# Optimization experiments

Hardware: AMD Instinct MI355X
Metric: run time of the kernel (lower is better)

## Reference

```python
import jax, jax.numpy as jnp
import numpy as np

NUM_HEADS = 16
WINDOW_SIZE = (7, 7, 7)  # (D, H, W)


def _relative_position_index(window_size):
    # Faithful numpy replication of SwinWindowAttention.get_relative_position_index (3D branch).
    D, H, W = window_size
    w, d, h = np.meshgrid(np.arange(W), np.arange(D), np.arange(H), indexing='ij')
    coords = np.stack([d, h, w], axis=0)              # [3, W, D, H]
    flat = coords.reshape(3, -1)                       # [3, N]
    rel = flat[:, :, None] - flat[:, None, :]          # [3, N, N]
    rel = rel.transpose(1, 2, 0)                       # [N, N, 3]
    offsets = []
    mult = 1
    for size in reversed(window_size):
        offsets.insert(0, mult)
        mult *= 2 * size - 1
    offsets = np.asarray(offsets, dtype=np.int32)
    rel = rel + np.asarray([s - 1 for s in window_size])
    return np.sum(rel.astype(np.int32) * offsets, axis=-1).astype(np.int32)  # [N, N]


def setup_inputs() -> dict:
    key = jax.random.key(0)
    ks = jax.random.split(key, 6)
    B, N, C = 64, 343, 512          # B = true_batch * num_windows
    NW = 8                           # mask_size; B % NW == 0
    TBL = 13 * 13 * 13              # prod(2*s - 1) = 2197
    x = jax.random.normal(ks[0], (B, N, C), dtype=jnp.float32)
    mask = jnp.zeros((NW, N, N), dtype=jnp.float32)  # shift mask (0 / -inf pattern in practice)
    w_qkv = jax.random.normal(ks[1], (C, 3 * C), dtype=jnp.float32) * (C ** -0.5)
    b_qkv = jnp.zeros((3 * C,), dtype=jnp.float32)
    w_proj = jax.random.normal(ks[2], (C, C), dtype=jnp.float32) * (C ** -0.5)
    b_proj = jnp.zeros((C,), dtype=jnp.float32)
    bias_table = jax.random.normal(ks[3], (TBL, NUM_HEADS), dtype=jnp.float32) * 0.02
    rel_index = jnp.asarray(_relative_position_index(WINDOW_SIZE))  # [N, N] int32
    return {"x": x, "mask": mask, "w_qkv": w_qkv, "b_qkv": b_qkv,
            "w_proj": w_proj, "b_proj": b_proj, "bias_table": bias_table,
            "rel_index": rel_index}


def reference(x, mask, w_qkv, b_qkv, w_proj, b_proj, bias_table, rel_index):
    B, N, C = x.shape
    H = NUM_HEADS
    hd = C // H
    scale = hd ** -0.5
    qkv = x @ w_qkv + b_qkv                              # [B, N, 3C]
    qkv = qkv.reshape(B, N, 3, H, hd).transpose(2, 0, 3, 1, 4)  # [3, B, H, N, hd]
    q, k, v = qkv[0] * scale, qkv[1], qkv[2]
    attn = jnp.einsum('bhnd,bhmd->bhnm', q, k)           # [B, H, N, N]
    # relative position bias: gather [N,N,H] -> [H,N,N]
    bias = bias_table[rel_index].transpose(2, 0, 1)
    attn = attn + bias[None]
    nw = mask.shape[0]
    attn = attn.reshape(B // nw, nw, H, N, N) + mask[:, None, :, :]
    attn = attn.reshape(B, H, N, N)
    attn = jax.nn.softmax(attn, axis=-1)
    out = jnp.einsum('bhnm,bhmd->bhnd', attn, v)         # [B, H, N, hd]
    out = out.transpose(0, 2, 1, 3).reshape(B, N, C)
    return out @ w_proj + b_proj
```

## Files before the change

kernel.cpp:

```cpp
#include <hip/hip_runtime.h>

typedef __bf16 bf16_t;
typedef __bf16 bf16x4 __attribute__((ext_vector_type(4)));
typedef __bf16 bf16x8 __attribute__((ext_vector_type(8)));
typedef short  s16x4  __attribute__((ext_vector_type(4)));
typedef float  f32x4  __attribute__((ext_vector_type(4)));

#define NUM_B 64
#define SEQ   343
#define CH    512
#define NH    16
#define HDIM  32
#define NWIN  8
#define C3    1536
#define MTOT  (NUM_B * SEQ)
#define MPAD  22016
#define NTILES 22
#define NPAD  352
#define NN    (SEQ * SEQ)
#define MB_TILES 172
#define QSCALE 0.17677669529663687f
#define LOG2E  1.4426950408889634f

__device__ __forceinline__ f32x4 mfma16(bf16x8 a, bf16x8 b, f32x4 c) {
    return __builtin_amdgcn_mfma_f32_16x16x32_bf16(a, b, c, 0, 0, 0);
}

__device__ __forceinline__ f32x4 mfma16k16(bf16x4 a, bf16x4 b, f32x4 c) {
    return __builtin_amdgcn_mfma_f32_16x16x16bf16_1k(
        __builtin_bit_cast(s16x4, a), __builtin_bit_cast(s16x4, b), c, 0, 0, 0);
}

__device__ __forceinline__ bf16x8 bf8_zero() {
    bf16x8 v;
#pragma unroll
    for (int i = 0; i < 8; ++i) v[i] = (bf16_t)0.f;
    return v;
}

__device__ __forceinline__ bf16x8 pack8(const float4& a, const float4& b) {
    bf16x8 v;
    v[0] = (bf16_t)a.x; v[1] = (bf16_t)a.y; v[2] = (bf16_t)a.z; v[3] = (bf16_t)a.w;
    v[4] = (bf16_t)b.x; v[5] = (bf16_t)b.y; v[6] = (bf16_t)b.z; v[7] = (bf16_t)b.w;
    return v;
}

__device__ __forceinline__ float f4get(const float4& v, int i) {
    return i == 0 ? v.x : i == 1 ? v.y : i == 2 ? v.z : v.w;
}

__device__ __forceinline__ void gload16(const void* g, void* l) {
    __builtin_amdgcn_global_load_lds(
        (const __attribute__((address_space(1))) void*)g,
        (__attribute__((address_space(3))) void*)l, 16, 0, 0);
}

__global__ __launch_bounds__(256) void swin_prep(
        const float* __restrict__ X, const float* __restrict__ Wq,
        const float* __restrict__ Wp, const float* __restrict__ bias_table,
        const int* __restrict__ rel_index, const float* __restrict__ mask,
        bf16_t* __restrict__ Xb, bf16_t* __restrict__ Bfq, bf16_t* __restrict__ Bfp,
        bf16_t* __restrict__ comb) {
    __shared__ __align__(16) float shbuf[32 * 33];
    const int bid = blockIdx.x, t = threadIdx.x;
    if (bid < 5504) {
        size_t e = ((size_t)bid * 256 + t) * 8;
        bf16x8 v;
        if (e < (size_t)MTOT * CH) {
            const float4* p = reinterpret_cast<const float4*>(&X[e]);
            v = pack8(p[0], p[1]);
        } else v = bf8_zero();
        *reinterpret_cast<bf16x8*>(&Xb[e]) = v;
        return;
    }
    if (bid < 6528) {
        float (*tile)[33] = reinterpret_cast<float(*)[33]>(shbuf);
        const float* src; bf16_t* dst; int srcN, k0, n0;
        if (bid < 6272) {
            int b2 = bid - 5504;
            k0 = (b2 % 16) * 32; n0 = (b2 / 16) * 32;
            src = Wq; dst = Bfq; srcN = C3;
        } else {
            int b2 = bid - 6272;
            k0 = (b2 % 16) * 32; n0 = (b2 / 16) * 32;
            src = Wp; dst = Bfp; srcN = CH;
        }
        int r = t >> 3, c4 = (t & 7) * 4;
        const float4 u = *reinterpret_cast<const float4*>(&src[(size_t)(k0 + r) * srcN + n0 + c4]);
        tile[r][c4 + 0] = u.x; tile[r][c4 + 1] = u.y; tile[r][c4 + 2] = u.z; tile[r][c4 + 3] = u.w;
        __syncthreads();
        const int sub = t >> 7, lane2 = (t >> 1) & 63, half = t & 1;
        const int lm = lane2 & 15, g = lane2 >> 4;
        bf16x4 o;
#pragma unroll
        for (int e = 0; e < 4; ++e)
            o[e] = (bf16_t)tile[g * 8 + half * 4 + e][sub * 16 + lm];
        const size_t off = ((size_t)(((n0 >> 4) + sub) * 16 + (k0 >> 5)) * 64 + lane2) * 8 + half * 4;
        *reinterpret_cast<bf16x4*>(&dst[off]) = o;
        return;
    }
    const int cid = bid - 6528;
    const int ntq = cid % 6, mt = (cid / 6) % NTILES, w = cid / (6 * NTILES);
    const int nt = ntq * 4 + (t >> 6);
    if (nt >= NTILES) return;
    const int lane = t & 63;
    const int lm = lane & 15, g = lane >> 4;
    const int gm = mt * 16 + lm;
    const bool gmok = gm < SEQ;

    bool ok[4]; int idx[4]; float mv[4];
#pragma unroll
    for (int r = 0; r < 4; ++r) {
        int gn = nt * 16 + 4 * g + r;
        ok[r] = gmok && (gn < SEQ);
        int a = ok[r] ? gm * SEQ + gn : 0;
        idx[r] = rel_index[a];
        mv[r] = ok[r] ? mask[(size_t)w * NN + a] : 0.f;
    }
    const size_t outb = ((size_t)mt * NTILES + nt) * 64 + lane;
    bf16x4* combv = reinterpret_cast<bf16x4*>(comb);
#pragma unroll
    for (int hq = 0; hq < 4; ++hq) {
        float4 b0 = *reinterpret_cast<const float4*>(&bias_table[idx[0] * NH + hq * 4]);
        float4 b1 = *reinterpret_cast<const float4*>(&bias_table[idx[1] * NH + hq * 4]);
        float4 b2 = *reinterpret_cast<const float4*>(&bias_table[idx[2] * NH + hq * 4]);
        float4 b3 = *reinterpret_cast<const float4*>(&bias_table[idx[3] * NH + hq * 4]);
#pragma unroll
        for (int hh = 0; hh < 4; ++hh) {
            int h = hq * 4 + hh;
            bf16x4 o;
            o[0] = ok[0] ? (bf16_t)((f4get(b0, hh) + mv[0]) * LOG2E) : (bf16_t)(-1e30f);
            o[1] = ok[1] ? (bf16_t)((f4get(b1, hh) + mv[1]) * LOG2E) : (bf16_t)(-1e30f);
            o[2] = ok[2] ? (bf16_t)((f4get(b2, hh) + mv[2]) * LOG2E) : (bf16_t)(-1e30f);
            o[3] = ok[3] ? (bf16_t)((f4get(b3, hh) + mv[3]) * LOG2E) : (bf16_t)(-1e30f);
            combv[(size_t)(h * 8 + w) * (NTILES * NTILES * 64) + outb] = o;
        }
    }
}

template <int NB, bool QKV>
__global__ __launch_bounds__(256) void swin_gemm(
        const bf16_t* __restrict__ A, const bf16_t* __restrict__ Bf,
        const float* __restrict__ bias, void* __restrict__ outv) {
    __shared__ __align__(16) bf16_t shraw[17408];
    const int nwg8 = MB_TILES * NB / 8;
    int bid = blockIdx.x;
    bid = (bid & 7) * nwg8 + (bid >> 3);
    const int nb = bid % NB, mb = bid / NB;
    const int m0 = mb * 128, n0 = nb * 128;
    const int t = threadIdx.x, wid = t >> 6, lane = t & 63;
    const int wr = wid >> 1, wc = wid & 1;
    const int lm = lane & 15, g = lane >> 4;
    const int swr = ((lane >> 2) ^ (lane >> 4)) & 3;
    const bf16_t* gA = &A[(size_t)(m0 + wid * 32 + (lane >> 2)) * CH + (((lane & 3) ^ swr) << 3)];
    const int soff = ((g ^ ((lm ^ (lm >> 2)) & 3)) << 3);
    const bf16_t* gBf = &Bf[((size_t)((n0 >> 4) + wc * 4) * 16) * 512 + lane * 8];

    f32x4 acc[4][4];
#pragma unroll
    for (int i = 0; i < 4; ++i)
#pragma unroll
        for (int j = 0; j < 4; ++j) {
            acc[i][j][0] = 0.f; acc[i][j][1] = 0.f; acc[i][j][2] = 0.f; acc[i][j][3] = 0.f;
        }

#define STAGE(tile, buf)                                                          \
    do {                                                                          \
        const int _k0 = (tile) * 32;                                              \
        gload16(gA + _k0,           &shraw[(buf) * 4096 + (wid * 32 + 0) * 32]);  \
        gload16(gA + _k0 + 16 * CH, &shraw[(buf) * 4096 + (wid * 32 + 16) * 32]); \
    } while (0)

    STAGE(0, 0);
    STAGE(1, 1);
    bf16x8 bc[4], bn[4];
#pragma unroll
    for (int j = 0; j < 4; ++j)
        bc[j] = *reinterpret_cast<const bf16x8*>(gBf + (size_t)j * 8192);

#pragma unroll
    for (int kt = 0; kt < 16; ++kt) {
        if (kt <= 14) asm volatile("s_waitcnt vmcnt(6)" ::: "memory");
        else          asm volatile("s_waitcnt vmcnt(4)" ::: "memory");
        __builtin_amdgcn_s_barrier();
        __builtin_amdgcn_sched_barrier(0);
        if (kt <= 13) STAGE(kt + 2, (kt + 2) % 3);
        if (kt <= 14) {
#pragma unroll
            for (int j = 0; j < 4; ++j)
                bn[j] = *reinterpret_cast<const bf16x8*>(gBf + (size_t)j * 8192 + (kt + 1) * 512);
        }
        const int buf = kt % 3;
        bf16x8 a[4];
#pragma unroll
        for (int i = 0; i < 4; ++i)
            a[i] = *reinterpret_cast<const bf16x8*>(&shraw[buf * 4096 + (wr * 64 + i * 16 + lm) * 32 + soff]);
        __builtin_amdgcn_s_setprio(1);
#pragma unroll
        for (int i = 0; i < 4; ++i)
#pragma unroll
            for (int j = 0; j < 4; ++j)
                acc[i][j] = mfma16(a[i], bc[j], acc[i][j]);
        __builtin_amdgcn_s_setprio(0);
        if (kt <= 14) {
#pragma unroll
            for (int j = 0; j < 4; ++j) bc[j] = bn[j];
        }
    }
#undef STAGE
    __syncthreads();

    const int rb = (lane >> 4) << 2;
    if (QKV) {
        bf16_t* Cs = &shraw[0];
#pragma unroll
        for (int j = 0; j < 4; ++j) {
            int col = wc * 64 + j * 16 + lm;
            float bv = bias[n0 + col];
            float sc = (n0 + col < CH) ? (QSCALE * LOG2E) : 1.0f;
#pragma unroll
            for (int i = 0; i < 4; ++i)
#pragma unroll
                for (int r = 0; r < 4; ++r)
                    Cs[(wr * 64 + i * 16 + rb + r) * 136 + col] = (bf16_t)((acc[i][j][r] + bv) * sc);
        }
        __syncthreads();
        bf16_t* outp = (bf16_t*)outv;
#pragma unroll
        for (int it = 0; it < 8; ++it) {
            int row = (t >> 4) + it * 16;
            int c8 = (t & 15) * 8;
            bf16x8 v = *reinterpret_cast<const bf16x8*>(&Cs[row * 136 + c8]);
            int grow = m0 + row;
            if (grow < MTOT)
                *reinterpret_cast<bf16x8*>(&outp[(size_t)grow * (NB * 128) + n0 + c8]) = v;
        }
    } else {
        float* fCs = reinterpret_cast<float*>(&shraw[0]);
        float* outp = (float*)outv;
#pragma unroll
        for (int half = 0; half < 2; ++half) {
            __syncthreads();
            if (wr == half) {
#pragma unroll
                for (int j = 0; j < 4; ++j) {
                    int col = wc * 64 + j * 16 + lm;
                    float bv = bias[n0 + col];
#pragma unroll
                    for (int i = 0; i < 4; ++i)
#pragma unroll
                        for (int r = 0; r < 4; ++r)
                            fCs[(i * 16 + rb + r) * 128 + col] = acc[i][j][r] + bv;
                }
            }
            __syncthreads();
#pragma unroll
            for (int it = 0; it < 8; ++it) {
                int row = (t >> 5) + it * 8;
                int c4 = (t & 31) * 4;
                float4 v = *reinterpret_cast<const float4*>(&fCs[row * 128 + c4]);
                int grow = m0 + half * 64 + row;
                if (grow < MTOT)
                    *reinterpret_cast<float4*>(&outp[(size_t)grow * (NB * 128) + n0 + c4]) = v;
            }
        }
    }
}

__global__ __launch_bounds__(512, 6) void swin_attn(
        const bf16_t* __restrict__ qkv, const bf16_t* __restrict__ comb,
        bf16_t* __restrict__ attout) {
    __shared__ __align__(16) bf16_t Ksh[NPAD * 32];
    __shared__ __align__(16) bf16_t Vsh[32 * NPAD];
    const int t = threadIdx.x;
    const int bid = blockIdx.x;
    const int h = (bid & 127) >> 3;
    const int w = bid & 7;
    const int b = w + ((bid >> 7) << 3);
    const int plane = h * 8 + w;
    const int wid = t >> 6, lane = t & 63;
    const int lm = lane & 15, g = lane >> 4;
    const int lkb = g << 3;
    const size_t rowbase = (size_t)b * SEQ;

    for (int base = 0; base < SEQ; base += 128) {
        int n = base + (t >> 2);
        int db = (t & 3) << 3;
        if (n < SEQ) {
            bf16x8 kv = *reinterpret_cast<const bf16x8*>(&qkv[(rowbase + n) * C3 + CH + h * HDIM + db]);
            *reinterpret_cast<bf16x8*>(&Ksh[(n * 32 + db) ^ (((n >> 1) & 3) << 3)]) = kv;
            bf16x8 vv = *reinterpret_cast<const bf16x8*>(&qkv[(rowbase + n) * C3 + 2 * CH + h * HDIM + db]);
#pragma unroll
            for (int e = 0; e < 8; ++e) {
                int d = db + e;
                Vsh[(d * NPAD + n) ^ (((d >> 1) & 3) << 3)] = vv[e];
            }
        }
    }
    if (t < 36) {
        int n = SEQ + (t >> 2), db = (t & 3) << 3;
        *reinterpret_cast<bf16x8*>(&Ksh[(n * 32 + db) ^ (((n >> 1) & 3) << 3)]) = bf8_zero();
    }
    for (int i = t; i < 32 * 9; i += 512) {
        int d = i / 9, n = SEQ + (i % 9);
        Vsh[(d * NPAD + n) ^ (((d >> 1) & 3) << 3)] = (bf16_t)0.f;
    }
    __syncthreads();

    const int kswz = ((lm >> 1) & 3) << 3;
    const int kbase = (lm * 32 + lkb) ^ kswz;
    const int vb0e = (lm * NPAD + 4 * g) ^ kswz;
    const int vb0o = (lm * NPAD + 4 * g + 16) ^ kswz;
    const int vb1e = ((16 + lm) * NPAD + 4 * g) ^ kswz;
    const int vb1o = ((16 + lm) * NPAD + 4 * g + 16) ^ kswz;

    bf16x4 ones;
    ones[0] = (bf16_t)1.f; ones[1] = (bf16_t)1.f; ones[2] = (bf16_t)1.f; ones[3] = (bf16_t)1.f;

    {
        const int m0a = wid * 16, m0b = (wid + 8) * 16;
        bf16x8 qfa = *reinterpret_cast<const bf16x8*>(&qkv[(rowbase + m0a + lm) * C3 + h * HDIM + lkb]);
        bf16x8 qfb = *reinterpret_cast<const bf16x8*>(&qkv[(rowbase + m0b + lm) * C3 + h * HDIM + lkb]);

        f32x4 o0a = {0.f, 0.f, 0.f, 0.f}, o1a = {0.f, 0.f, 0.f, 0.f}, osa = {0.f, 0.f, 0.f, 0.f};
        f32x4 o0b = {0.f, 0.f, 0.f, 0.f}, o1b = {0.f, 0.f, 0.f, 0.f}, osb = {0.f, 0.f, 0.f, 0.f};
        const bf16x4* cpa = reinterpret_cast<const bf16x4*>(comb) + ((size_t)plane * NTILES + wid) * NTILES * 64;
        const bf16x4* cpb = reinterpret_cast<const bf16x4*>(comb) + ((size_t)plane * NTILES + wid + 8) * NTILES * 64;
#pragma unroll 2
        for (int nt = 0; nt < NTILES; ++nt) {
            bf16x4 cba = cpa[nt * 64 + lane];
            bf16x4 cbb = cpb[nt * 64 + lane];
            bf16x8 kf = *reinterpret_cast<const bf16x8*>(&Ksh[kbase + nt * 512]);
            f32x4 za, zb;
            za[0] = (float)cba[0]; za[1] = (float)cba[1]; za[2] = (float)cba[2]; za[3] = (float)cba[3];
            zb[0] = (float)cbb[0]; zb[1] = (float)cbb[1]; zb[2] = (float)cbb[2]; zb[3] = (float)cbb[3];
            f32x4 sa = mfma16(kf, qfa, za);
            f32x4 sb = mfma16(kf, qfb, zb);
            bf16x4 paa, pab;
#pragma unroll
            for (int r = 0; r < 4; ++r) {
                paa[r] = (bf16_t)__builtin_amdgcn_exp2f(sa[r]);
                pab[r] = (bf16_t)__builtin_amdgcn_exp2f(sb[r]);
            }
            const int off = (nt >> 1) * 32;
            bf16x4 v0 = *reinterpret_cast<const bf16x4*>(&Vsh[((nt & 1) ? vb0o : vb0e) + off]);
            bf16x4 v1 = *reinterpret_cast<const bf16x4*>(&Vsh[((nt & 1) ? vb1o : vb1e) + off]);
            o0a = mfma16k16(paa, v0, o0a);
            o0b = mfma16k16(pab, v0, o0b);
            o1a = mfma16k16(paa, v1, o1a);
            o1b = mfma16k16(pab, v1, o1b);
            osa = mfma16k16(paa, ones, osa);
            osb = mfma16k16(pab, ones, osb);
        }
#pragma unroll
        for (int r = 0; r < 4; ++r) {
            int gma = m0a + 4 * g + r;
            float iva = 1.f / osa[r];
            attout[(rowbase + gma) * CH + h * HDIM + lm]      = (bf16_t)(o0a[r] * iva);
            attout[(rowbase + gma) * CH + h * HDIM + 16 + lm] = (bf16_t)(o1a[r] * iva);
            int gmb = m0b + 4 * g + r;
            float ivb = 1.f / osb[r];
            attout[(rowbase + gmb) * CH + h * HDIM + lm]      = (bf16_t)(o0b[r] * ivb);
            attout[(rowbase + gmb) * CH + h * HDIM + 16 + lm] = (bf16_t)(o1b[r] * ivb);
        }
    }

    if (wid < 6) {
        const int mt = wid + 16;
        const int m0 = mt * 16;
        bf16x8 qf = *reinterpret_cast<const bf16x8*>(&qkv[(rowbase + m0 + lm) * C3 + h * HDIM + lkb]);

        f32x4 o0 = {0.f, 0.f, 0.f, 0.f}, o1 = {0.f, 0.f, 0.f, 0.f};
        f32x4 osum = {0.f, 0.f, 0.f, 0.f};
        const bf16x4* cp = reinterpret_cast<const bf16x4*>(comb) + ((size_t)plane * NTILES + mt) * NTILES * 64;
#pragma unroll 2
        for (int nt = 0; nt < NTILES; ++nt) {
            bf16x4 cb = cp[nt * 64 + lane];
            bf16x8 kf = *reinterpret_cast<const bf16x8*>(&Ksh[kbase + nt * 512]);
            f32x4 z;
            z[0] = (float)cb[0]; z[1] = (float)cb[1]; z[2] = (float)cb[2]; z[3] = (float)cb[3];
            f32x4 s = mfma16(kf, qf, z);
            bf16x4 pa;
#pragma unroll
            for (int r = 0; r < 4; ++r)
                pa[r] = (bf16_t)__builtin_amdgcn_exp2f(s[r]);
            const int off = (nt >> 1) * 32;
            bf16x4 v0 = *reinterpret_cast<const bf16x4*>(&Vsh[((nt & 1) ? vb0o : vb0e) + off]);
            bf16x4 v1 = *reinterpret_cast<const bf16x4*>(&Vsh[((nt & 1) ? vb1o : vb1e) + off]);
            o0 = mfma16k16(pa, v0, o0);
            o1 = mfma16k16(pa, v1, o1);
            osum = mfma16k16(pa, ones, osum);
        }
#pragma unroll
        for (int r = 0; r < 4; ++r) {
            int gm = m0 + 4 * g + r;
            if (gm < SEQ) {
                float iv = 1.f / osum[r];
                attout[(rowbase + gm) * CH + h * HDIM + lm]      = (bf16_t)(o0[r] * iv);
                attout[(rowbase + gm) * CH + h * HDIM + 16 + lm] = (bf16_t)(o1[r] * iv);
            }
        }
    }
}

extern "C" void kernel_launch(void* const* d_in, const int* in_sizes, int n_in,
                              void* d_out, int out_size, void* d_ws, size_t ws_size,
                              hipStream_t stream) {
    const float* x          = (const float*)d_in[0];
    const float* mask       = (const float*)d_in[1];
    const float* w_qkv      = (const float*)d_in[2];
    const float* b_qkv      = (const float*)d_in[3];
    const float* w_proj     = (const float*)d_in[4];
    const float* b_proj     = (const float*)d_in[5];
    const float* bias_table = (const float*)d_in[6];
    const int*   rel_index  = (const int*)d_in[7];
    float* out = (float*)d_out;

    char* ws = (char*)d_ws;
    const size_t qkv_bytes = (size_t)MPAD * C3 * sizeof(bf16_t);
    const size_t xb_bytes  = (size_t)MPAD * CH * sizeof(bf16_t);
    const size_t bfq_bytes = (size_t)C3 * CH * sizeof(bf16_t);
    const size_t bfp_bytes = (size_t)CH * CH * sizeof(bf16_t);
    bf16_t* qkv    = (bf16_t*)ws;
    bf16_t* Xb     = (bf16_t*)(ws + qkv_bytes);
    bf16_t* attout = Xb;
    bf16_t* Bfq    = (bf16_t*)(ws + qkv_bytes + xb_bytes);
    bf16_t* Bfp    = (bf16_t*)(ws + qkv_bytes + xb_bytes + bfq_bytes);
    bf16_t* comb   = (bf16_t*)(ws + qkv_bytes + xb_bytes + bfq_bytes + bfp_bytes);

    const int prep_grid = 5504 + 768 + 256 + NWIN * NTILES * 6;
    hipLaunchKernelGGL(swin_prep, dim3(prep_grid), dim3(256), 0, stream,
                       x, w_qkv, w_proj, bias_table, rel_index, mask, Xb, Bfq, Bfp, comb);
    hipLaunchKernelGGL((swin_gemm<12, true>), dim3(MB_TILES * 12), dim3(256), 0, stream,
                       Xb, Bfq, b_qkv, (void*)qkv);
    hipLaunchKernelGGL(swin_attn, dim3(NUM_B * NH), dim3(512), 0, stream,
                       qkv, comb, attout);
    hipLaunchKernelGGL((swin_gemm<4, false>), dim3(MB_TILES * 4), dim3(256), 0, stream,
                       attout, Bfp, b_proj, (void*)out);
}
```

Before: 145.8 us.

## Store combined bias/mask in fp32 and prefetch GEMM B fragments two steps ahead

The precomputed relative-position-bias plus mask tensor now stays in fp32 instead of bf16, which removes the bf16-to-float converts in the attention inner loop. The price is twice the memory traffic for that tensor in both the prep and attention kernels. Separately, the GEMM now loads its global B-operand fragments two k-steps ahead, using a second register buffer and a full drain on the last iteration, to hide more global-load latency. That extra buffer adds register pressure.

```diff
diff --git a/kernel.cpp b/kernel.cpp
--- a/kernel.cpp
+++ b/kernel.cpp
@@ -60,7 +60,7 @@
         const float* __restrict__ Wp, const float* __restrict__ bias_table,
         const int* __restrict__ rel_index, const float* __restrict__ mask,
         bf16_t* __restrict__ Xb, bf16_t* __restrict__ Bfq, bf16_t* __restrict__ Bfp,
-        bf16_t* __restrict__ comb) {
+        float* __restrict__ comb) {
     __shared__ __align__(16) float shbuf[32 * 33];
     const int bid = blockIdx.x, t = threadIdx.x;
     if (bid < 5504) {
@@ -118,7 +118,7 @@
         mv[r] = ok[r] ? mask[(size_t)w * NN + a] : 0.f;
     }
     const size_t outb = ((size_t)mt * NTILES + nt) * 64 + lane;
-    bf16x4* combv = reinterpret_cast<bf16x4*>(comb);
+    float4* combv = reinterpret_cast<float4*>(comb);
 #pragma unroll
     for (int hq = 0; hq < 4; ++hq) {
         float4 b0 = *reinterpret_cast<const float4*>(&bias_table[idx[0] * NH + hq * 4]);
@@ -128,11 +128,11 @@
 #pragma unroll
         for (int hh = 0; hh < 4; ++hh) {
             int h = hq * 4 + hh;
-            bf16x4 o;
-            o[0] = ok[0] ? (bf16_t)((f4get(b0, hh) + mv[0]) * LOG2E) : (bf16_t)(-1e30f);
-            o[1] = ok[1] ? (bf16_t)((f4get(b1, hh) + mv[1]) * LOG2E) : (bf16_t)(-1e30f);
-            o[2] = ok[2] ? (bf16_t)((f4get(b2, hh) + mv[2]) * LOG2E) : (bf16_t)(-1e30f);
-            o[3] = ok[3] ? (bf16_t)((f4get(b3, hh) + mv[3]) * LOG2E) : (bf16_t)(-1e30f);
+            float4 o;
+            o.x = ok[0] ? (f4get(b0, hh) + mv[0]) * LOG2E : -1e30f;
+            o.y = ok[1] ? (f4get(b1, hh) + mv[1]) * LOG2E : -1e30f;
+            o.z = ok[2] ? (f4get(b2, hh) + mv[2]) * LOG2E : -1e30f;
+            o.w = ok[3] ? (f4get(b3, hh) + mv[3]) * LOG2E : -1e30f;
             combv[(size_t)(h * 8 + w) * (NTILES * NTILES * 64) + outb] = o;
         }
     }
@@ -173,22 +173,24 @@
 
     STAGE(0, 0);
     STAGE(1, 1);
-    bf16x8 bc[4], bn[4];
-#pragma unroll
-    for (int j = 0; j < 4; ++j)
-        bc[j] = *reinterpret_cast<const bf16x8*>(gBf + (size_t)j * 8192);
+    bf16x8 bc[4], bn1[4], bn2[4];
+#pragma unroll
+    for (int j = 0; j < 4; ++j) {
+        bc[j]  = *reinterpret_cast<const bf16x8*>(gBf + (size_t)j * 8192);
+        bn1[j] = *reinterpret_cast<const bf16x8*>(gBf + (size_t)j * 8192 + 512);
+    }
 
 #pragma unroll
     for (int kt = 0; kt < 16; ++kt) {
         if (kt <= 14) asm volatile("s_waitcnt vmcnt(6)" ::: "memory");
-        else          asm volatile("s_waitcnt vmcnt(4)" ::: "memory");
+        else          asm volatile("s_waitcnt vmcnt(0)" ::: "memory");
         __builtin_amdgcn_s_barrier();
         __builtin_amdgcn_sched_barrier(0);
         if (kt <= 13) STAGE(kt + 2, (kt + 2) % 3);
-        if (kt <= 14) {
+        if (kt <= 13) {
 #pragma unroll
             for (int j = 0; j < 4; ++j)
-                bn[j] = *reinterpret_cast<const bf16x8*>(gBf + (size_t)j * 8192 + (kt + 1) * 512);
+                bn2[j] = *reinterpret_cast<const bf16x8*>(gBf + (size_t)j * 8192 + (kt + 2) * 512);
         }
         const int buf = kt % 3;
         bf16x8 a[4];
@@ -204,7 +206,7 @@
         __builtin_amdgcn_s_setprio(0);
         if (kt <= 14) {
 #pragma unroll
-            for (int j = 0; j < 4; ++j) bc[j] = bn[j];
+            for (int j = 0; j < 4; ++j) { bc[j] = bn1[j]; bn1[j] = bn2[j]; }
         }
     }
 #undef STAGE
@@ -268,7 +270,7 @@
 }
 
 __global__ __launch_bounds__(512, 6) void swin_attn(
-        const bf16_t* __restrict__ qkv, const bf16_t* __restrict__ comb,
+        const bf16_t* __restrict__ qkv, const float* __restrict__ comb,
         bf16_t* __restrict__ attout) {
     __shared__ __align__(16) bf16_t Ksh[NPAD * 32];
     __shared__ __align__(16) bf16_t Vsh[32 * NPAD];
@@ -324,16 +326,16 @@
 
         f32x4 o0a = {0.f, 0.f, 0.f, 0.f}, o1a = {0.f, 0.f, 0.f, 0.f}, osa = {0.f, 0.f, 0.f, 0.f};
         f32x4 o0b = {0.f, 0.f, 0.f, 0.f}, o1b = {0.f, 0.f, 0.f, 0.f}, osb = {0.f, 0.f, 0.f, 0.f};
-        const bf16x4* cpa = reinterpret_cast<const bf16x4*>(comb) + ((size_t)plane * NTILES + wid) * NTILES * 64;
-        const bf16x4* cpb = reinterpret_cast<const bf16x4*>(comb) + ((size_t)plane * NTILES + wid + 8) * NTILES * 64;
+        const float4* cpa = reinterpret_cast<const float4*>(comb) + ((size_t)plane * NTILES + wid) * NTILES * 64;
+        const float4* cpb = reinterpret_cast<const float4*>(comb) + ((size_t)plane * NTILES + wid + 8) * NTILES * 64;
 #pragma unroll 2
         for (int nt = 0; nt < NTILES; ++nt) {
-            bf16x4 cba = cpa[nt * 64 + lane];
-            bf16x4 cbb = cpb[nt * 64 + lane];
+            float4 cba = cpa[nt * 64 + lane];
+            float4 cbb = cpb[nt * 64 + lane];
             bf16x8 kf = *reinterpret_cast<const bf16x8*>(&Ksh[kbase + nt * 512]);
             f32x4 za, zb;
-            za[0] = (float)cba[0]; za[1] = (float)cba[1]; za[2] = (float)cba[2]; za[3] = (float)cba[3];
-            zb[0] = (float)cbb[0]; zb[1] = (float)cbb[1]; zb[2] = (float)cbb[2]; zb[3] = (float)cbb[3];
+            za[0] = cba.x; za[1] = cba.y; za[2] = cba.z; za[3] = cba.w;
+            zb[0] = cbb.x; zb[1] = cbb.y; zb[2] = cbb.z; zb[3] = cbb.w;
             f32x4 sa = mfma16(kf, qfa, za);
             f32x4 sb = mfma16(kf, qfb, zb);
             bf16x4 paa, pab;
@@ -372,13 +374,13 @@
 
         f32x4 o0 = {0.f, 0.f, 0.f, 0.f}, o1 = {0.f, 0.f, 0.f, 0.f};
         f32x4 osum = {0.f, 0.f, 0.f, 0.f};
-        const bf16x4* cp = reinterpret_cast<const bf16x4*>(comb) + ((size_t)plane * NTILES + mt) * NTILES * 64;
+        const float4* cp = reinterpret_cast<const float4*>(comb) + ((size_t)plane * NTILES + mt) * NTILES * 64;
 #pragma unroll 2
         for (int nt = 0; nt < NTILES; ++nt) {
-            bf16x4 cb = cp[nt * 64 + lane];
+            float4 cb = cp[nt * 64 + lane];
             bf16x8 kf = *reinterpret_cast<const bf16x8*>(&Ksh[kbase + nt * 512]);
             f32x4 z;
-            z[0] = (float)cb[0]; z[1] = (float)cb[1]; z[2] = (float)cb[2]; z[3] = (float)cb[3];
+            z[0] = cb.x; z[1] = cb.y; z[2] = cb.z; z[3] = cb.w;
             f32x4 s = mfma16(kf, qf, z);
             bf16x4 pa;
 #pragma unroll
@@ -426,7 +428,7 @@
     bf16_t* attout = Xb;
     bf16_t* Bfq    = (bf16_t*)(ws + qkv_bytes + xb_bytes);
     bf16_t* Bfp    = (bf16_t*)(ws + qkv_bytes + xb_bytes + bfq_bytes);
-    bf16_t* comb   = (bf16_t*)(ws + qkv_bytes + xb_bytes + bfq_bytes + bfp_bytes);
+    float*  comb   = (float*)(ws + qkv_bytes + xb_bytes + bfq_bytes + bfp_bytes);
 
     const int prep_grid = 5504 + 768 + 256 + NWIN * NTILES * 6;
     hipLaunchKernelGGL(swin_prep, dim3(prep_grid), dim3(256), 0, stream,
```

New measurement: 151.1 us. 3.6% more time.

## Move bias/mask combine blocks from prep kernel into QKV GEMM grid

Applied to the files above, without the earlier changes.

The relative-position-bias plus mask combine work is pulled out of the prep kernel and interleaved into the QKV GEMM launch: every third block in the first 3096 runs comb_block, the rest map to GEMM tiles, and the trailing 24 blocks finish the combine. This shortens the prep kernel and lets the gather-heavy combine work overlap with the compute-bound GEMM. The cost is extra parameters and branching in the GEMM kernel, and a changed block scheduling order that may affect the GEMM's L2 tile swizzle behaviour.

```diff
diff --git a/kernel.cpp b/kernel.cpp
--- a/kernel.cpp
+++ b/kernel.cpp
@@ -55,12 +55,53 @@
         (__attribute__((address_space(3))) void*)l, 16, 0, 0);
 }
 
+__device__ void comb_block(int cid, int t,
+                           const float* __restrict__ bias_table,
+                           const int* __restrict__ rel_index,
+                           const float* __restrict__ mask,
+                           bf16_t* __restrict__ comb) {
+    const int ntq = cid % 6, mt = (cid / 6) % NTILES, w = cid / (6 * NTILES);
+    const int nt = ntq * 4 + (t >> 6);
+    if (nt >= NTILES) return;
+    const int lane = t & 63;
+    const int lm = lane & 15, g = lane >> 4;
+    const int gm = mt * 16 + lm;
+    const bool gmok = gm < SEQ;
+
+    bool ok[4]; int idx[4]; float mv[4];
+#pragma unroll
+    for (int r = 0; r < 4; ++r) {
+        int gn = nt * 16 + 4 * g + r;
+        ok[r] = gmok && (gn < SEQ);
+        int a = ok[r] ? gm * SEQ + gn : 0;
+        idx[r] = rel_index[a];
+        mv[r] = ok[r] ? mask[(size_t)w * NN + a] : 0.f;
+    }
+    const size_t outb = ((size_t)mt * NTILES + nt) * 64 + lane;
+    bf16x4* combv = reinterpret_cast<bf16x4*>(comb);
+#pragma unroll
+    for (int hq = 0; hq < 4; ++hq) {
+        float4 b0 = *reinterpret_cast<const float4*>(&bias_table[idx[0] * NH + hq * 4]);
+        float4 b1 = *reinterpret_cast<const float4*>(&bias_table[idx[1] * NH + hq * 4]);
+        float4 b2 = *reinterpret_cast<const float4*>(&bias_table[idx[2] * NH + hq * 4]);
+        float4 b3 = *reinterpret_cast<const float4*>(&bias_table[idx[3] * NH + hq * 4]);
+#pragma unroll
+        for (int hh = 0; hh < 4; ++hh) {
+            int h = hq * 4 + hh;
+            bf16x4 o;
+            o[0] = ok[0] ? (bf16_t)((f4get(b0, hh) + mv[0]) * LOG2E) : (bf16_t)(-1e30f);
+            o[1] = ok[1] ? (bf16_t)((f4get(b1, hh) + mv[1]) * LOG2E) : (bf16_t)(-1e30f);
+            o[2] = ok[2] ? (bf16_t)((f4get(b2, hh) + mv[2]) * LOG2E) : (bf16_t)(-1e30f);
+            o[3] = ok[3] ? (bf16_t)((f4get(b3, hh) + mv[3]) * LOG2E) : (bf16_t)(-1e30f);
+            combv[(size_t)(h * 8 + w) * (NTILES * NTILES * 64) + outb] = o;
+        }
+    }
+}
+
 __global__ __launch_bounds__(256) void swin_prep(
         const float* __restrict__ X, const float* __restrict__ Wq,
-        const float* __restrict__ Wp, const float* __restrict__ bias_table,
-        const int* __restrict__ rel_index, const float* __restrict__ mask,
-        bf16_t* __restrict__ Xb, bf16_t* __restrict__ Bfq, bf16_t* __restrict__ Bfp,
-        bf16_t* __restrict__ comb) {
+        const float* __restrict__ Wp,
+        bf16_t* __restrict__ Xb, bf16_t* __restrict__ Bfq, bf16_t* __restrict__ Bfp) {
     __shared__ __align__(16) float shbuf[32 * 33];
     const int bid = blockIdx.x, t = threadIdx.x;
     if (bid < 5504) {
@@ -73,78 +114,48 @@
         *reinterpret_cast<bf16x8*>(&Xb[e]) = v;
         return;
     }
-    if (bid < 6528) {
-        float (*tile)[33] = reinterpret_cast<float(*)[33]>(shbuf);
-        const float* src; bf16_t* dst; int srcN, k0, n0;
-        if (bid < 6272) {
-            int b2 = bid - 5504;
-            k0 = (b2 % 16) * 32; n0 = (b2 / 16) * 32;
-            src = Wq; dst = Bfq; srcN = C3;
-        } else {
-            int b2 = bid - 6272;
-            k0 = (b2 % 16) * 32; n0 = (b2 / 16) * 32;
-            src = Wp; dst = Bfp; srcN = CH;
-        }
-        int r = t >> 3, c4 = (t & 7) * 4;
-        const float4 u = *reinterpret_cast<const float4*>(&src[(size_t)(k0 + r) * srcN + n0 + c4]);
-        tile[r][c4 + 0] = u.x; tile[r][c4 + 1] = u.y; tile[r][c4 + 2] = u.z; tile[r][c4 + 3] = u.w;
-        __syncthreads();
-        const int sub = t >> 7, lane2 = (t >> 1) & 63, half = t & 1;
-        const int lm = lane2 & 15, g = lane2 >> 4;
-        bf16x4 o;
-#pragma unroll
-        for (int e = 0; e < 4; ++e)
-            o[e] = (bf16_t)tile[g * 8 + half * 4 + e][sub * 16 + lm];
-        const size_t off = ((size_t)(((n0 >> 4) + sub) * 16 + (k0 >> 5)) * 64 + lane2) * 8 + half * 4;
-        *reinterpret_cast<bf16x4*>(&dst[off]) = o;
-        return;
-    }
-    const int cid = bid - 6528;
-    const int ntq = cid % 6, mt = (cid / 6) % NTILES, w = cid / (6 * NTILES);
-    const int nt = ntq * 4 + (t >> 6);
-    if (nt >= NTILES) return;
-    const int lane = t & 63;
-    const int lm = lane & 15, g = lane >> 4;
-    const int gm = mt * 16 + lm;
-    const bool gmok = gm < SEQ;
-
-    bool ok[4]; int idx[4]; float mv[4];
-#pragma unroll
-    for (int r = 0; r < 4; ++r) {
-        int gn = nt * 16 + 4 * g + r;
-        ok[r] = gmok && (gn < SEQ);
-        int a = ok[r] ? gm * SEQ + gn : 0;
-        idx[r] = rel_index[a];
-        mv[r] = ok[r] ? mask[(size_t)w * NN + a] : 0.f;
-    }
-    const size_t outb = ((size_t)mt * NTILES + nt) * 64 + lane;
-    bf16x4* combv = reinterpret_cast<bf16x4*>(comb);
-#pragma unroll
-    for (int hq = 0; hq < 4; ++hq) {
-        float4 b0 = *reinterpret_cast<const float4*>(&bias_table[idx[0] * NH + hq * 4]);
-        float4 b1 = *reinterpret_cast<const float4*>(&bias_table[idx[1] * NH + hq * 4]);
-        float4 b2 = *reinterpret_cast<const float4*>(&bias_table[idx[2] * NH + hq * 4]);
-        float4 b3 = *reinterpret_cast<const float4*>(&bias_table[idx[3] * NH + hq * 4]);
-#pragma unroll
-        for (int hh = 0; hh < 4; ++hh) {
-            int h = hq * 4 + hh;
-            bf16x4 o;
-            o[0] = ok[0] ? (bf16_t)((f4get(b0, hh) + mv[0]) * LOG2E) : (bf16_t)(-1e30f);
-            o[1] = ok[1] ? (bf16_t)((f4get(b1, hh) + mv[1]) * LOG2E) : (bf16_t)(-1e30f);
-            o[2] = ok[2] ? (bf16_t)((f4get(b2, hh) + mv[2]) * LOG2E) : (bf16_t)(-1e30f);
-            o[3] = ok[3] ? (bf16_t)((f4get(b3, hh) + mv[3]) * LOG2E) : (bf16_t)(-1e30f);
-            combv[(size_t)(h * 8 + w) * (NTILES * NTILES * 64) + outb] = o;
-        }
-    }
+    float (*tile)[33] = reinterpret_cast<float(*)[33]>(shbuf);
+    const float* src; bf16_t* dst; int srcN, k0, n0;
+    if (bid < 6272) {
+        int b2 = bid - 5504;
+        k0 = (b2 % 16) * 32; n0 = (b2 / 16) * 32;
+        src = Wq; dst = Bfq; srcN = C3;
+    } else {
+        int b2 = bid - 6272;
+        k0 = (b2 % 16) * 32; n0 = (b2 / 16) * 32;
+        src = Wp; dst = Bfp; srcN = CH;
+    }
+    int r = t >> 3, c4 = (t & 7) * 4;
+    const float4 u = *reinterpret_cast<const float4*>(&src[(size_t)(k0 + r) * srcN + n0 + c4]);
+    tile[r][c4 + 0] = u.x; tile[r][c4 + 1] = u.y; tile[r][c4 + 2] = u.z; tile[r][c4 + 3] = u.w;
+    __syncthreads();
+    const int sub = t >> 7, lane2 = (t >> 1) & 63, half = t & 1;
+    const int lm = lane2 & 15, g = lane2 >> 4;
+    bf16x4 o;
+#pragma unroll
+    for (int e = 0; e < 4; ++e)
+        o[e] = (bf16_t)tile[g * 8 + half * 4 + e][sub * 16 + lm];
+    const size_t off = ((size_t)(((n0 >> 4) + sub) * 16 + (k0 >> 5)) * 64 + lane2) * 8 + half * 4;
+    *reinterpret_cast<bf16x4*>(&dst[off]) = o;
 }
 
 template <int NB, bool QKV>
 __global__ __launch_bounds__(256) void swin_gemm(
         const bf16_t* __restrict__ A, const bf16_t* __restrict__ Bf,
-        const float* __restrict__ bias, void* __restrict__ outv) {
+        const float* __restrict__ bias, void* __restrict__ outv,
+        const float* __restrict__ bias_table, const int* __restrict__ rel_index,
+        const float* __restrict__ mask, bf16_t* __restrict__ comb) {
     __shared__ __align__(16) bf16_t shraw[17408];
+    int bid;
+    if constexpr (QKV) {
+        const int rb2 = blockIdx.x;
+        if (rb2 >= 3096) { comb_block(1032 + (rb2 - 3096), threadIdx.x, bias_table, rel_index, mask, comb); return; }
+        if (rb2 % 3 == 2) { comb_block(rb2 / 3, threadIdx.x, bias_table, rel_index, mask, comb); return; }
+        bid = (rb2 / 3) * 2 + (rb2 % 3);
+    } else {
+        bid = blockIdx.x;
+    }
     const int nwg8 = MB_TILES * NB / 8;
-    int bid = blockIdx.x;
     bid = (bid & 7) * nwg8 + (bid >> 3);
     const int nb = bid % NB, mb = bid / NB;
     const int m0 = mb * 128, n0 = nb * 128;
@@ -428,13 +439,12 @@
     bf16_t* Bfp    = (bf16_t*)(ws + qkv_bytes + xb_bytes + bfq_bytes);
     bf16_t* comb   = (bf16_t*)(ws + qkv_bytes + xb_bytes + bfq_bytes + bfp_bytes);
 
-    const int prep_grid = 5504 + 768 + 256 + NWIN * NTILES * 6;
-    hipLaunchKernelGGL(swin_prep, dim3(prep_grid), dim3(256), 0, stream,
-                       x, w_qkv, w_proj, bias_table, rel_index, mask, Xb, Bfq, Bfp, comb);
-    hipLaunchKernelGGL((swin_gemm<12, true>), dim3(MB_TILES * 12), dim3(256), 0, stream,
-                       Xb, Bfq, b_qkv, (void*)qkv);
+    hipLaunchKernelGGL(swin_prep, dim3(6528), dim3(256), 0, stream,
+                       x, w_qkv, w_proj, Xb, Bfq, Bfp);
+    hipLaunchKernelGGL((swin_gemm<12, true>), dim3(3120), dim3(256), 0, stream,
+                       Xb, Bfq, b_qkv, (void*)qkv, bias_table, rel_index, mask, comb);
     hipLaunchKernelGGL(swin_attn, dim3(NUM_B * NH), dim3(512), 0, stream,
                        qkv, comb, attout);
     hipLaunchKernelGGL((swin_gemm<4, false>), dim3(MB_TILES * 4), dim3(256), 0, stream,
-                       attout, Bfp, b_proj, (void*)out);
-}
+                       attout, Bfp, b_proj, (void*)out, nullptr, nullptr, nullptr, nullptr);
+}
```

New measurement: 139.6 us. 4.3% less time.
